# Optimization experiments

Measured on AMD Instinct MI355X. Metric: run time of the kernel, lower is better.

The kernel has to match this reference:

```python
import jax, jax.numpy as jnp
import numpy as np

B, S, D = 8, 2048, 1024
H = 2 * D  # FFN hidden
EPS = 1e-5

def _layernorm(x, gamma, beta):
    mu = jnp.mean(x, axis=-1, keepdims=True)
    var = jnp.mean(jnp.square(x - mu), axis=-1, keepdims=True)
    return (x - mu) * jax.lax.rsqrt(var + EPS) * gamma + beta

def setup_inputs() -> dict:
    key = jax.random.key(0)
    ks = jax.random.split(key, 9)
    s = 1.0 / np.sqrt(D)
    x = jax.random.normal(ks[0], (B, S, D), dtype=jnp.float32)
    Wq = jax.random.uniform(ks[1], (D, D), jnp.float32, -s, s)
    Wk = jax.random.uniform(ks[2], (D, D), jnp.float32, -s, s)
    Wv = jax.random.uniform(ks[3], (D, D), jnp.float32, -s, s)
    W1 = jax.random.uniform(ks[4], (H, D), jnp.float32, -s, s)
    b1 = jax.random.uniform(ks[5], (H,), jnp.float32, -s, s)
    s2 = 1.0 / np.sqrt(H)
    W2 = jax.random.uniform(ks[6], (D, H), jnp.float32, -s2, s2)
    b2 = jax.random.uniform(ks[7], (D,), jnp.float32, -s2, s2)
    g1 = jnp.ones((D,), jnp.float32); be1 = jnp.zeros((D,), jnp.float32)
    g2 = jnp.ones((D,), jnp.float32); be2 = jnp.zeros((D,), jnp.float32)
    return {"x": x, "Wq": Wq, "Wk": Wk, "Wv": Wv, "W1": W1, "b1": b1,
            "W2": W2, "b2": b2, "g1": g1, "be1": be1, "g2": g2, "be2": be2}

def reference(x, Wq, Wk, Wv, W1, b1, W2, b2, g1, be1, g2, be2):
    # q/k/v projections (torch Linear: x @ W.T)
    q = jnp.einsum('bsd,ed->bse', x, Wq)
    k = jnp.einsum('bsd,ed->bse', x, Wk)
    v = jnp.einsum('bsd,ed->bse', x, Wv)
    scores = jnp.einsum('bqd,bkd->bqk', q, k) / jnp.sqrt(jnp.float32(D))
    attn = jax.nn.softmax(scores, axis=-1)
    attn_out = jnp.einsum('bqk,bkd->bqd', attn, v)
    h = _layernorm(x + attn_out, g1, be1)
    ff = jnp.einsum('bsh,dh->bsd', jax.nn.relu(jnp.einsum('bsd,hd->bsh', h, W1) + b1), W2) + b2
    return _layernorm(h + ff, g2, be2)
```

## Files before the change

### kernel.cpp

```cpp
#include <hip/hip_runtime.h>
#include <hip/hip_bf16.h>


typedef __attribute__((ext_vector_type(4))) float  f32x4;
typedef __attribute__((ext_vector_type(8))) short  short8;
typedef __attribute__((ext_vector_type(4))) short  short4v;
typedef __attribute__((ext_vector_type(8))) __bf16 bf16x8;
typedef unsigned short ushort_t;

static __device__ __forceinline__ unsigned short f2bf(float f) {
  unsigned u = __builtin_bit_cast(unsigned, f);
  u += 0x7fffu + ((u >> 16) & 1u);
  return (unsigned short)(u >> 16);
}
static __device__ __forceinline__ float bf2f(unsigned short u) {
  return __builtin_bit_cast(float, (unsigned)u << 16);
}

#define GLDS16(g, l)                                                        \
  __builtin_amdgcn_global_load_lds(                                         \
      (const __attribute__((address_space(1))) void*)(g),                   \
      (__attribute__((address_space(3))) void*)(l), 16, 0, 0)

__global__ __launch_bounds__(256) void cvt_f32_bf16(
    const float* __restrict__ in, ushort_t* __restrict__ out, long n) {
  long i = ((long)blockIdx.x * 256 + threadIdx.x) * 8;
  if (i >= n) return;
  f32x4 a = *(const f32x4*)(in + i);
  f32x4 b = *(const f32x4*)(in + i + 4);
  short8 t;
  t[0] = (short)f2bf(a.x); t[1] = (short)f2bf(a.y);
  t[2] = (short)f2bf(a.z); t[3] = (short)f2bf(a.w);
  t[4] = (short)f2bf(b.x); t[5] = (short)f2bf(b.y);
  t[6] = (short)f2bf(b.z); t[7] = (short)f2bf(b.w);
  *(short8*)(out + i) = t;
}

enum { EP_QKV = 0, EP_BF16 = 1, EP_PV = 2, EP_FF1 = 3, EP_FF2 = 4 };

constexpr long BSDc = 8L * 2048 * 1024;

template <int EPI>
__global__ __launch_bounds__(512, 2) void gemm_bt(
    const ushort_t* __restrict__ A, const ushort_t* __restrict__ B,
    void* __restrict__ C, int N, int K, long sA, long sB, long sC, long sRes,
    const float* __restrict__ bias, const float* __restrict__ res,
    float scale) {
  __shared__ __align__(16) ushort_t As[2][2][8192];
  __shared__ __align__(16) ushort_t Bs[2][2][8192];
  const int tid  = threadIdx.x;
  const int lane = tid & 63;
  const int w    = tid >> 6;
  const int wm   = w >> 2;
  const int wn   = w & 3;
  const int l15  = lane & 15;
  const int hi   = lane >> 4;
  const long bz  = blockIdx.z;
  const long m0  = (long)blockIdx.x * 256;
  const long n0  = (long)blockIdx.y * 256;
  const ushort_t* Ab = A + bz * sA;
  const ushort_t* Bb = B + bz * sB;

  const int srow = tid >> 3;
  const int sc   = (tid & 7) ^ (srow & 7);
  const long offA0 = (m0 + srow) * (long)K + sc * 8;
  const long offB0 = (n0 + srow) * (long)K + sc * 8;
  const int dst0 = w * 512;
  const int dst1 = 4096 + w * 512;

#define STAGE_A(t, h)                                                       \
  {                                                                         \
    const long o_ = (long)(t) * 64 + (long)(h) * 128 * K;                   \
    ushort_t* l_ = &As[(t) & 1][h][0];                                      \
    GLDS16(Ab + offA0 + o_, l_ + dst0);                                     \
    GLDS16(Ab + offA0 + 64 * (long)K + o_, l_ + dst1);                      \
  }
#define STAGE_B(t, h)                                                       \
  {                                                                         \
    const long o_ = (long)(t) * 64 + (long)(h) * 128 * K;                   \
    ushort_t* l_ = &Bs[(t) & 1][h][0];                                      \
    GLDS16(Bb + offB0 + o_, l_ + dst0);                                     \
    GLDS16(Bb + offB0 + 64 * (long)K + o_, l_ + dst1);                      \
  }

  const int ab0 = l15 * 128 + ((hi) ^ (l15 & 7)) * 16;
  const int ab1 = l15 * 128 + ((4 + hi) ^ (l15 & 7)) * 16;

#define READ_A(ai)                                                          \
  _Pragma("unroll") for (int i = 0; i < 4; ++i) {                           \
    afr[i][0] = *(const short8*)(Ah + (ai) * 8192 + i * 2048 + ab0);        \
    afr[i][1] = *(const short8*)(Ah + (ai) * 8192 + i * 2048 + ab1);        \
  }
#define READ_B(bj)                                                          \
  _Pragma("unroll") for (int j = 0; j < 2; ++j) {                           \
    bfr[bj][j][0] = *(const short8*)(Bh + (bj) * 4096 + j * 2048 + ab0);    \
    bfr[bj][j][1] = *(const short8*)(Bh + (bj) * 4096 + j * 2048 + ab1);    \
  }
#define QMFMA(ib, jb, bsel)                                                 \
  _Pragma("unroll") for (int i = 0; i < 4; ++i)                             \
  _Pragma("unroll") for (int j = 0; j < 2; ++j)                             \
  _Pragma("unroll") for (int ks = 0; ks < 2; ++ks)                          \
    acc[(ib) + i][(jb) + j] = __builtin_amdgcn_mfma_f32_16x16x32_bf16(      \
        __builtin_bit_cast(bf16x8, afr[i][ks]),                             \
        __builtin_bit_cast(bf16x8, bfr[bsel][j][ks]),                       \
        acc[(ib) + i][(jb) + j], 0, 0, 0);

  f32x4 acc[8][4] = {};
  const int NT = K >> 6;

  STAGE_B(0, 0) STAGE_B(0, 1) STAGE_A(0, 0) STAGE_A(0, 1)
  STAGE_B(1, 0) STAGE_B(1, 1)
  asm volatile("s_waitcnt vmcnt(4)" ::: "memory");
  __builtin_amdgcn_sched_barrier(0);
  __builtin_amdgcn_s_barrier();
  __builtin_amdgcn_sched_barrier(0);

  for (int u = 0; u < NT; ++u) {
    const int d = u & 1;
    const char* Ah = (const char*)&As[d][wm][0];
    const char* Bh = (const char*)&Bs[d][wn >> 1][0] + (wn & 1) * 8192;
    short8 afr[4][2], bfr[2][2][2];
    READ_A(0)
    READ_B(0)
    if (u + 1 < NT) STAGE_A(u + 1, 0)
    __builtin_amdgcn_s_setprio(1);
    QMFMA(0, 0, 0)
    __builtin_amdgcn_s_setprio(0);
    READ_B(1)
    if (u + 1 < NT) STAGE_A(u + 1, 1)
    __builtin_amdgcn_s_setprio(1);
    QMFMA(0, 2, 1)
    __builtin_amdgcn_s_setprio(0);
    __builtin_amdgcn_s_barrier();
    READ_A(1)
    if (u + 2 < NT) STAGE_B(u + 2, 0)
    __builtin_amdgcn_s_setprio(1);
    QMFMA(4, 2, 1)
    __builtin_amdgcn_s_setprio(0);
    if (u + 2 < NT) STAGE_B(u + 2, 1)
    __builtin_amdgcn_s_setprio(1);
    QMFMA(4, 0, 0)
    __builtin_amdgcn_s_setprio(0);
    if (u + 1 < NT) {
      if (u + 2 < NT) {
        asm volatile("s_waitcnt vmcnt(4)" ::: "memory");
      } else {
        asm volatile("s_waitcnt vmcnt(0)" ::: "memory");
      }
      __builtin_amdgcn_sched_barrier(0);
      __builtin_amdgcn_s_barrier();
      __builtin_amdgcn_sched_barrier(0);
    }
  }
#undef STAGE_A
#undef STAGE_B
#undef READ_A
#undef READ_B
#undef QMFMA

  const int rb0 = hi << 2;
  const int cl  = l15;
#pragma unroll
  for (int i = 0; i < 8; ++i) {
#pragma unroll
    for (int j = 0; j < 4; ++j) {
      long gmb = m0 + wm * 128 + i * 16 + rb0;
      long gc  = n0 + wn * 64 + j * 16 + cl;
      if constexpr (EPI == EP_QKV) {
        long which = gc >> 10;
        long col   = gc & 1023;
        if (which == 2) {
          long bb = gmb >> 11, s = gmb & 2047;
          short4v pk;
#pragma unroll
          for (int r = 0; r < 4; ++r) pk[r] = (short)f2bf(acc[i][j][r]);
          *(short4v*)((ushort_t*)C + 2 * BSDc + ((bb << 10) + col) * 2048 + s) =
              pk;
        } else {
#pragma unroll
          for (int r = 0; r < 4; ++r)
            ((ushort_t*)C)[which * BSDc + (gmb + r) * 1024 + col] =
                f2bf(acc[i][j][r]);
        }
      } else {
#pragma unroll
        for (int r = 0; r < 4; ++r) {
          long gm = gmb + r;
          float v = acc[i][j][r] * scale;
          if constexpr (EPI == EP_BF16) {
            ((ushort_t*)C)[bz * sC + gm * N + gc] = f2bf(v);
          } else if constexpr (EPI == EP_PV) {
            v += res[bz * sRes + gm * N + gc];
            ((float*)C)[bz * sC + gm * N + gc] = v;
          } else if constexpr (EPI == EP_FF1) {
            v += bias[gc];
            v = v > 0.f ? v : 0.f;
            ((ushort_t*)C)[gm * N + gc] = f2bf(v);
          } else {
            v += bias[gc] + res[gm * N + gc];
            ((float*)C)[gm * N + gc] = v;
          }
        }
      }
    }
  }
}

__global__ __launch_bounds__(256) void softmax_inplace(
    ushort_t* __restrict__ P) {
  __shared__ float rmax[4], rsum[4];
  const int tid   = threadIdx.x;
  const long base = (long)blockIdx.x * 2048;
  short8 sv = *(const short8*)(P + base + tid * 8);
  float v[8];
#pragma unroll
  for (int j = 0; j < 8; ++j) v[j] = bf2f((unsigned short)sv[j]);
  float mx = v[0];
#pragma unroll
  for (int j = 1; j < 8; ++j) mx = fmaxf(mx, v[j]);
#pragma unroll
  for (int off = 32; off; off >>= 1) mx = fmaxf(mx, __shfl_down(mx, off, 64));
  if ((tid & 63) == 0) rmax[tid >> 6] = mx;
  __syncthreads();
  mx = fmaxf(fmaxf(rmax[0], rmax[1]), fmaxf(rmax[2], rmax[3]));
  float s = 0.f;
#pragma unroll
  for (int j = 0; j < 8; ++j) {
    v[j] = __expf(v[j] - mx);
    s += v[j];
  }
#pragma unroll
  for (int off = 32; off; off >>= 1) s += __shfl_down(s, off, 64);
  if ((tid & 63) == 0) rsum[tid >> 6] = s;
  __syncthreads();
  s = (rsum[0] + rsum[1]) + (rsum[2] + rsum[3]);
  float inv = 1.f / s;
  short8 o;
#pragma unroll
  for (int j = 0; j < 8; ++j) o[j] = (short)f2bf(v[j] * inv);
  *(short8*)(P + base + tid * 8) = o;
}

template <int MODE>
__global__ __launch_bounds__(256) void ln_row(const float* __restrict__ X,
                                              const float* __restrict__ g,
                                              const float* __restrict__ be,
                                              float* __restrict__ Yf,
                                              ushort_t* __restrict__ Yb) {
  __shared__ float rs[4], rq[4];
  const int tid   = threadIdx.x;
  const long base = (long)blockIdx.x << 10;
  f32x4 v = *(const f32x4*)(X + base + tid * 4);
  float s = v.x + v.y + v.z + v.w;
  float q = v.x * v.x + v.y * v.y + v.z * v.z + v.w * v.w;
#pragma unroll
  for (int off = 32; off; off >>= 1) {
    s += __shfl_down(s, off, 64);
    q += __shfl_down(q, off, 64);
  }
  if ((tid & 63) == 0) {
    rs[tid >> 6] = s;
    rq[tid >> 6] = q;
  }
  __syncthreads();
  s = (rs[0] + rs[1]) + (rs[2] + rs[3]);
  q = (rq[0] + rq[1]) + (rq[2] + rq[3]);
  float mu   = s * (1.f / 1024.f);
  float var  = q * (1.f / 1024.f) - mu * mu;
  float rstd = rsqrtf(var + 1e-5f);
  int c    = tid * 4;
  f32x4 gg = *(const f32x4*)(g + c);
  f32x4 bb = *(const f32x4*)(be + c);
  f32x4 y;
  y.x = (v.x - mu) * rstd * gg.x + bb.x;
  y.y = (v.y - mu) * rstd * gg.y + bb.y;
  y.z = (v.z - mu) * rstd * gg.z + bb.z;
  y.w = (v.w - mu) * rstd * gg.w + bb.w;
  *(f32x4*)(Yf + base + c) = y;
  if constexpr (MODE == 0) {
    short4v ob;
    ob[0] = (short)f2bf(y.x);
    ob[1] = (short)f2bf(y.y);
    ob[2] = (short)f2bf(y.z);
    ob[3] = (short)f2bf(y.w);
    *(short4v*)(Yb + base + c) = ob;
  }
}

extern "C" void kernel_launch(void* const* d_in, const int* in_sizes, int n_in,
                              void* d_out, int out_size, void* d_ws,
                              size_t ws_size, hipStream_t stream) {
  const float* x   = (const float*)d_in[0];
  const float* Wq  = (const float*)d_in[1];
  const float* Wk  = (const float*)d_in[2];
  const float* Wv  = (const float*)d_in[3];
  const float* W1  = (const float*)d_in[4];
  const float* b1  = (const float*)d_in[5];
  const float* W2  = (const float*)d_in[6];
  const float* b2  = (const float*)d_in[7];
  const float* g1  = (const float*)d_in[8];
  const float* be1 = (const float*)d_in[9];
  const float* g2  = (const float*)d_in[10];
  const float* be2 = (const float*)d_in[11];
  float* out = (float*)d_out;

  constexpr long BSD = 8L * 2048 * 1024;
  constexpr long BSS = 8L * 2048 * 2048;
  constexpr long DD  = 1024L * 1024;
  constexpr long HD  = 2048L * 1024;

  ushort_t* qb  = (ushort_t*)d_ws;
  ushort_t* kb  = qb + BSD;
  ushort_t* vTb = kb + BSD;
  ushort_t* sP  = vTb + BSD;
  float*    r1  = (float*)(sP + BSS);

  ushort_t* xb    = sP;
  ushort_t* Wqkvb = (ushort_t*)r1;
  ushort_t* W1b   = kb;
  ushort_t* W2b   = kb + HD;
  ushort_t* hb    = qb;
  float*    h     = out;

  dim3 blk(256), gblk(512);
  const long SD = 2048L * 1024, SS = 2048L * 2048, DS = 1024L * 2048;

  cvt_f32_bf16<<<dim3(8192), blk, 0, stream>>>(x, xb, BSD);
  cvt_f32_bf16<<<dim3(512), blk, 0, stream>>>(Wq, Wqkvb, DD);
  cvt_f32_bf16<<<dim3(512), blk, 0, stream>>>(Wk, Wqkvb + DD, DD);
  cvt_f32_bf16<<<dim3(512), blk, 0, stream>>>(Wv, Wqkvb + 2 * DD, DD);
  gemm_bt<EP_QKV><<<dim3(64, 12, 1), gblk, 0, stream>>>(
      xb, Wqkvb, qb, 3072, 1024, 0, 0, 0, 0, nullptr, nullptr, 1.f);
  gemm_bt<EP_BF16><<<dim3(8, 8, 8), gblk, 0, stream>>>(
      qb, kb, sP, 2048, 1024, SD, SD, SS, 0, nullptr, nullptr, 0.03125f);
  cvt_f32_bf16<<<dim3(1024), blk, 0, stream>>>(W1, W1b, HD);
  cvt_f32_bf16<<<dim3(1024), blk, 0, stream>>>(W2, W2b, HD);
  softmax_inplace<<<dim3(16384), blk, 0, stream>>>(sP);
  gemm_bt<EP_PV><<<dim3(8, 4, 8), gblk, 0, stream>>>(
      sP, vTb, r1, 1024, 2048, SS, DS, SD, SD, nullptr, x, 1.f);
  ln_row<0><<<dim3(16384), blk, 0, stream>>>(r1, g1, be1, h, hb);
  gemm_bt<EP_FF1><<<dim3(64, 8, 1), gblk, 0, stream>>>(
      hb, W1b, sP, 2048, 1024, 0, 0, 0, 0, b1, nullptr, 1.f);
  gemm_bt<EP_FF2><<<dim3(64, 4, 1), gblk, 0, stream>>>(
      sP, W2b, r1, 1024, 2048, 0, 0, 0, 0, b2, h, 1.f);
  ln_row<1><<<dim3(16384), blk, 0, stream>>>(r1, g2, be2, out, nullptr);
}
```

Baseline: 494.1 us.

## Switch GEMM inner loop from 16x16x32 to 32x32x16 bf16 MFMA tiles

Replaces the 16x16x32 bf16 MFMA instructions with 32x32x16 ones and rewrites the LDS fragment reads and the swizzle offsets to match the 32-row operand layout. It also remaps the epilogue to the 32x32 accumulator layout, where each lane holds 4 groups of 4 rows. Larger MFMA tiles cut the LDS reads per FLOP and the number of issued instructions. In exchange, each of the fewer wider instructions has a longer latency and the accumulator layout changes.

```diff
diff --git a/kernel.cpp b/kernel.cpp
--- a/kernel.cpp
+++ b/kernel.cpp
@@ -2,10 +2,11 @@
 #include <hip/hip_bf16.h>
 
 
-typedef __attribute__((ext_vector_type(4))) float  f32x4;
-typedef __attribute__((ext_vector_type(8))) short  short8;
-typedef __attribute__((ext_vector_type(4))) short  short4v;
-typedef __attribute__((ext_vector_type(8))) __bf16 bf16x8;
+typedef __attribute__((ext_vector_type(4))) float   f32x4;
+typedef __attribute__((ext_vector_type(16))) float  f32x16;
+typedef __attribute__((ext_vector_type(8))) short   short8;
+typedef __attribute__((ext_vector_type(4))) short   short4v;
+typedef __attribute__((ext_vector_type(8))) __bf16  bf16x8;
 typedef unsigned short ushort_t;
 
 static __device__ __forceinline__ unsigned short f2bf(float f) {
@@ -53,8 +54,9 @@
   const int w    = tid >> 6;
   const int wm   = w >> 2;
   const int wn   = w & 3;
-  const int l15  = lane & 15;
-  const int hi   = lane >> 4;
+  const int l31  = lane & 31;
+  const int hi1  = lane >> 5;
+  const int e    = lane & 7;
   const long bz  = blockIdx.z;
   const long m0  = (long)blockIdx.x * 256;
   const long n0  = (long)blockIdx.y * 256;
@@ -83,29 +85,28 @@
     GLDS16(Bb + offB0 + 64 * (long)K + o_, l_ + dst1);                      \
   }
 
-  const int ab0 = l15 * 128 + ((hi) ^ (l15 & 7)) * 16;
-  const int ab1 = l15 * 128 + ((4 + hi) ^ (l15 & 7)) * 16;
-
-#define READ_A(ai)                                                          \
-  _Pragma("unroll") for (int i = 0; i < 4; ++i) {                           \
-    afr[i][0] = *(const short8*)(Ah + (ai) * 8192 + i * 2048 + ab0);        \
-    afr[i][1] = *(const short8*)(Ah + (ai) * 8192 + i * 2048 + ab1);        \
-  }
-#define READ_B(bj)                                                          \
-  _Pragma("unroll") for (int j = 0; j < 2; ++j) {                           \
-    bfr[bj][j][0] = *(const short8*)(Bh + (bj) * 4096 + j * 2048 + ab0);    \
-    bfr[bj][j][1] = *(const short8*)(Bh + (bj) * 4096 + j * 2048 + ab1);    \
-  }
-#define QMFMA(ib, jb, bsel)                                                 \
-  _Pragma("unroll") for (int i = 0; i < 4; ++i)                             \
-  _Pragma("unroll") for (int j = 0; j < 2; ++j)                             \
-  _Pragma("unroll") for (int ks = 0; ks < 2; ++ks)                          \
-    acc[(ib) + i][(jb) + j] = __builtin_amdgcn_mfma_f32_16x16x32_bf16(      \
+  int sks[4];
+#pragma unroll
+  for (int ks = 0; ks < 4; ++ks) sks[ks] = (((2 * ks + hi1) ^ e) << 4);
+
+#define READ_A2(tb)                                                         \
+  _Pragma("unroll") for (int i = 0; i < 2; ++i)                             \
+  _Pragma("unroll") for (int ks = 0; ks < 4; ++ks)                          \
+    afr[i][ks] = *(const short8*)(Ah + (((tb) + i) * 32 + l31) * 128 +      \
+                                  sks[ks]);
+#define READ_B1(bj)                                                         \
+  _Pragma("unroll") for (int ks = 0; ks < 4; ++ks)                          \
+    bfr[bj][ks] = *(const short8*)(Bh + ((bj) * 32 + l31) * 128 + sks[ks]);
+
+#define QMFMA(ig, jt)                                                       \
+  _Pragma("unroll") for (int ks = 0; ks < 4; ++ks)                          \
+  _Pragma("unroll") for (int i = 0; i < 2; ++i)                             \
+    acc[(ig) * 2 + i][jt] = __builtin_amdgcn_mfma_f32_32x32x16_bf16(        \
         __builtin_bit_cast(bf16x8, afr[i][ks]),                             \
-        __builtin_bit_cast(bf16x8, bfr[bsel][j][ks]),                       \
-        acc[(ib) + i][(jb) + j], 0, 0, 0);
-
-  f32x4 acc[8][4] = {};
+        __builtin_bit_cast(bf16x8, bfr[jt][ks]), acc[(ig) * 2 + i][jt], 0,  \
+        0, 0);
+
+  f32x16 acc[4][2] = {};
   const int NT = K >> 6;
 
   STAGE_B(0, 0) STAGE_B(0, 1) STAGE_A(0, 0) STAGE_A(0, 1)
@@ -119,27 +120,27 @@
     const int d = u & 1;
     const char* Ah = (const char*)&As[d][wm][0];
     const char* Bh = (const char*)&Bs[d][wn >> 1][0] + (wn & 1) * 8192;
-    short8 afr[4][2], bfr[2][2][2];
-    READ_A(0)
-    READ_B(0)
+    short8 afr[2][4], bfr[2][4];
+    READ_A2(0)
+    READ_B1(0)
     if (u + 1 < NT) STAGE_A(u + 1, 0)
     __builtin_amdgcn_s_setprio(1);
-    QMFMA(0, 0, 0)
+    QMFMA(0, 0)
     __builtin_amdgcn_s_setprio(0);
-    READ_B(1)
+    READ_B1(1)
     if (u + 1 < NT) STAGE_A(u + 1, 1)
     __builtin_amdgcn_s_setprio(1);
-    QMFMA(0, 2, 1)
+    QMFMA(0, 1)
     __builtin_amdgcn_s_setprio(0);
     __builtin_amdgcn_s_barrier();
-    READ_A(1)
+    READ_A2(2)
     if (u + 2 < NT) STAGE_B(u + 2, 0)
     __builtin_amdgcn_s_setprio(1);
-    QMFMA(4, 2, 1)
+    QMFMA(1, 1)
     __builtin_amdgcn_s_setprio(0);
     if (u + 2 < NT) STAGE_B(u + 2, 1)
     __builtin_amdgcn_s_setprio(1);
-    QMFMA(4, 0, 0)
+    QMFMA(1, 0)
     __builtin_amdgcn_s_setprio(0);
     if (u + 1 < NT) {
       if (u + 2 < NT) {
@@ -154,51 +155,54 @@
   }
 #undef STAGE_A
 #undef STAGE_B
-#undef READ_A
-#undef READ_B
+#undef READ_A2
+#undef READ_B1
 #undef QMFMA
 
-  const int rb0 = hi << 2;
-  const int cl  = l15;
-#pragma unroll
-  for (int i = 0; i < 8; ++i) {
-#pragma unroll
-    for (int j = 0; j < 4; ++j) {
-      long gmb = m0 + wm * 128 + i * 16 + rb0;
-      long gc  = n0 + wn * 64 + j * 16 + cl;
-      if constexpr (EPI == EP_QKV) {
-        long which = gc >> 10;
-        long col   = gc & 1023;
-        if (which == 2) {
-          long bb = gmb >> 11, s = gmb & 2047;
-          short4v pk;
-#pragma unroll
-          for (int r = 0; r < 4; ++r) pk[r] = (short)f2bf(acc[i][j][r]);
-          *(short4v*)((ushort_t*)C + 2 * BSDc + ((bb << 10) + col) * 2048 + s) =
-              pk;
+#pragma unroll
+  for (int it = 0; it < 4; ++it) {
+#pragma unroll
+    for (int jt = 0; jt < 2; ++jt) {
+      const long rowb = m0 + wm * 128 + it * 32;
+      const long gc   = n0 + wn * 64 + jt * 32 + l31;
+#pragma unroll
+      for (int q = 0; q < 4; ++q) {
+        const long gr0 = rowb + 8 * q + 4 * hi1;
+        if constexpr (EPI == EP_QKV) {
+          long which = gc >> 10;
+          long col   = gc & 1023;
+          if (which == 2) {
+            long bb = gr0 >> 11, s = gr0 & 2047;
+            short4v pk;
+#pragma unroll
+            for (int r = 0; r < 4; ++r)
+              pk[r] = (short)f2bf(acc[it][jt][q * 4 + r]);
+            *(short4v*)((ushort_t*)C + 2 * BSDc + ((bb << 10) + col) * 2048 +
+                        s) = pk;
+          } else {
+#pragma unroll
+            for (int r = 0; r < 4; ++r)
+              ((ushort_t*)C)[which * BSDc + (gr0 + r) * 1024 + col] =
+                  f2bf(acc[it][jt][q * 4 + r]);
+          }
         } else {
 #pragma unroll
-          for (int r = 0; r < 4; ++r)
-            ((ushort_t*)C)[which * BSDc + (gmb + r) * 1024 + col] =
-                f2bf(acc[i][j][r]);
-        }
-      } else {
-#pragma unroll
-        for (int r = 0; r < 4; ++r) {
-          long gm = gmb + r;
-          float v = acc[i][j][r] * scale;
-          if constexpr (EPI == EP_BF16) {
-            ((ushort_t*)C)[bz * sC + gm * N + gc] = f2bf(v);
-          } else if constexpr (EPI == EP_PV) {
-            v += res[bz * sRes + gm * N + gc];
-            ((float*)C)[bz * sC + gm * N + gc] = v;
-          } else if constexpr (EPI == EP_FF1) {
-            v += bias[gc];
-            v = v > 0.f ? v : 0.f;
-            ((ushort_t*)C)[gm * N + gc] = f2bf(v);
-          } else {
-            v += bias[gc] + res[gm * N + gc];
-            ((float*)C)[gm * N + gc] = v;
+          for (int r = 0; r < 4; ++r) {
+            long gm = gr0 + r;
+            float v = acc[it][jt][q * 4 + r] * scale;
+            if constexpr (EPI == EP_BF16) {
+              ((ushort_t*)C)[bz * sC + gm * N + gc] = f2bf(v);
+            } else if constexpr (EPI == EP_PV) {
+              v += res[bz * sRes + gm * N + gc];
+              ((float*)C)[bz * sC + gm * N + gc] = v;
+            } else if constexpr (EPI == EP_FF1) {
+              v += bias[gc];
+              v = v > 0.f ? v : 0.f;
+              ((ushort_t*)C)[gm * N + gc] = f2bf(v);
+            } else {
+              v += bias[gc] + res[gm * N + gc];
+              ((float*)C)[gm * N + gc] = v;
+            }
           }
         }
       }
```

New measurement: 548.3 us. 1.11x slower.

## Use 1024-thread GEMM blocks with 16 waves each owning 64x64 tile

Applied to the files above, without the earlier changes.

The GEMM block grows from 512 to 1024 threads (16 waves), so each wave computes a 64x64 sub-tile instead of 128x64. Accumulator registers per wave are halved and each thread issues one global-to-LDS load per stage instead of two, with the vmcnt waits adjusted to match. The 256x256 block tile and LDS footprint stay the same. Occupancy drops to one block per CU, and each wave now loads its A fragment once per k-step with less MFMA work to hide that load behind. More waves also means more contention at the barriers.

```diff
diff --git a/kernel.cpp b/kernel.cpp
--- a/kernel.cpp
+++ b/kernel.cpp
@@ -41,7 +41,7 @@
 constexpr long BSDc = 8L * 2048 * 1024;
 
 template <int EPI>
-__global__ __launch_bounds__(512, 2) void gemm_bt(
+__global__ __launch_bounds__(1024, 1) void gemm_bt(
     const ushort_t* __restrict__ A, const ushort_t* __restrict__ B,
     void* __restrict__ C, int N, int K, long sA, long sB, long sC, long sRes,
     const float* __restrict__ bias, const float* __restrict__ res,
@@ -51,8 +51,8 @@
   const int tid  = threadIdx.x;
   const int lane = tid & 63;
   const int w    = tid >> 6;
-  const int wm   = w >> 2;
-  const int wn   = w & 3;
+  const int wm2  = w >> 2;
+  const int wn2  = w & 3;
   const int l15  = lane & 15;
   const int hi   = lane >> 4;
   const long bz  = blockIdx.z;
@@ -65,85 +65,71 @@
   const int sc   = (tid & 7) ^ (srow & 7);
   const long offA0 = (m0 + srow) * (long)K + sc * 8;
   const long offB0 = (n0 + srow) * (long)K + sc * 8;
-  const int dst0 = w * 512;
-  const int dst1 = 4096 + w * 512;
+  const int dst = (w << 9);
 
 #define STAGE_A(t, h)                                                       \
-  {                                                                         \
-    const long o_ = (long)(t) * 64 + (long)(h) * 128 * K;                   \
-    ushort_t* l_ = &As[(t) & 1][h][0];                                      \
-    GLDS16(Ab + offA0 + o_, l_ + dst0);                                     \
-    GLDS16(Ab + offA0 + 64 * (long)K + o_, l_ + dst1);                      \
-  }
+  GLDS16(Ab + offA0 + (long)(t) * 64 + (long)(h) * 128 * K,                 \
+         &As[(t) & 1][h][0] + dst);
 #define STAGE_B(t, h)                                                       \
-  {                                                                         \
-    const long o_ = (long)(t) * 64 + (long)(h) * 128 * K;                   \
-    ushort_t* l_ = &Bs[(t) & 1][h][0];                                      \
-    GLDS16(Bb + offB0 + o_, l_ + dst0);                                     \
-    GLDS16(Bb + offB0 + 64 * (long)K + o_, l_ + dst1);                      \
-  }
+  GLDS16(Bb + offB0 + (long)(t) * 64 + (long)(h) * 128 * K,                 \
+         &Bs[(t) & 1][h][0] + dst);
 
   const int ab0 = l15 * 128 + ((hi) ^ (l15 & 7)) * 16;
   const int ab1 = l15 * 128 + ((4 + hi) ^ (l15 & 7)) * 16;
 
-#define READ_A(ai)                                                          \
+#define READ_A_ALL                                                          \
   _Pragma("unroll") for (int i = 0; i < 4; ++i) {                           \
-    afr[i][0] = *(const short8*)(Ah + (ai) * 8192 + i * 2048 + ab0);        \
-    afr[i][1] = *(const short8*)(Ah + (ai) * 8192 + i * 2048 + ab1);        \
-  }
-#define READ_B(bj)                                                          \
-  _Pragma("unroll") for (int j = 0; j < 2; ++j) {                           \
-    bfr[bj][j][0] = *(const short8*)(Bh + (bj) * 4096 + j * 2048 + ab0);    \
-    bfr[bj][j][1] = *(const short8*)(Bh + (bj) * 4096 + j * 2048 + ab1);    \
-  }
-#define QMFMA(ib, jb, bsel)                                                 \
+    afr[i][0] = *(const short8*)(Ah + i * 2048 + ab0);                      \
+    afr[i][1] = *(const short8*)(Ah + i * 2048 + ab1);                      \
+  }
+#define READ_B2(bj0)                                                        \
+  _Pragma("unroll") for (int jj = 0; jj < 2; ++jj) {                        \
+    bfr[jj][0] = *(const short8*)(Bh + ((bj0) + jj) * 2048 + ab0);          \
+    bfr[jj][1] = *(const short8*)(Bh + ((bj0) + jj) * 2048 + ab1);          \
+  }
+#define QMFMA(jb)                                                           \
   _Pragma("unroll") for (int i = 0; i < 4; ++i)                             \
-  _Pragma("unroll") for (int j = 0; j < 2; ++j)                             \
+  _Pragma("unroll") for (int jj = 0; jj < 2; ++jj)                          \
   _Pragma("unroll") for (int ks = 0; ks < 2; ++ks)                          \
-    acc[(ib) + i][(jb) + j] = __builtin_amdgcn_mfma_f32_16x16x32_bf16(      \
+    acc[i][(jb) + jj] = __builtin_amdgcn_mfma_f32_16x16x32_bf16(            \
         __builtin_bit_cast(bf16x8, afr[i][ks]),                             \
-        __builtin_bit_cast(bf16x8, bfr[bsel][j][ks]),                       \
-        acc[(ib) + i][(jb) + j], 0, 0, 0);
-
-  f32x4 acc[8][4] = {};
+        __builtin_bit_cast(bf16x8, bfr[jj][ks]), acc[i][(jb) + jj], 0, 0,   \
+        0);
+
+  f32x4 acc[4][4] = {};
   const int NT = K >> 6;
 
   STAGE_B(0, 0) STAGE_B(0, 1) STAGE_A(0, 0) STAGE_A(0, 1)
   STAGE_B(1, 0) STAGE_B(1, 1)
-  asm volatile("s_waitcnt vmcnt(4)" ::: "memory");
+  asm volatile("s_waitcnt vmcnt(2)" ::: "memory");
   __builtin_amdgcn_sched_barrier(0);
   __builtin_amdgcn_s_barrier();
   __builtin_amdgcn_sched_barrier(0);
 
   for (int u = 0; u < NT; ++u) {
     const int d = u & 1;
-    const char* Ah = (const char*)&As[d][wm][0];
-    const char* Bh = (const char*)&Bs[d][wn >> 1][0] + (wn & 1) * 8192;
-    short8 afr[4][2], bfr[2][2][2];
-    READ_A(0)
-    READ_B(0)
+    const char* Ah = (const char*)&As[d][wm2 >> 1][0] + (wm2 & 1) * 8192;
+    const char* Bh = (const char*)&Bs[d][wn2 >> 1][0] + (wn2 & 1) * 8192;
+    short8 afr[4][2], bfr[2][2];
+    READ_A_ALL
+    READ_B2(0)
     if (u + 1 < NT) STAGE_A(u + 1, 0)
     __builtin_amdgcn_s_setprio(1);
-    QMFMA(0, 0, 0)
+    QMFMA(0)
     __builtin_amdgcn_s_setprio(0);
-    READ_B(1)
+    READ_B2(2)
     if (u + 1 < NT) STAGE_A(u + 1, 1)
     __builtin_amdgcn_s_setprio(1);
-    QMFMA(0, 2, 1)
+    QMFMA(2)
     __builtin_amdgcn_s_setprio(0);
     __builtin_amdgcn_s_barrier();
-    READ_A(1)
-    if (u + 2 < NT) STAGE_B(u + 2, 0)
-    __builtin_amdgcn_s_setprio(1);
-    QMFMA(4, 2, 1)
-    __builtin_amdgcn_s_setprio(0);
-    if (u + 2 < NT) STAGE_B(u + 2, 1)
-    __builtin_amdgcn_s_setprio(1);
-    QMFMA(4, 0, 0)
-    __builtin_amdgcn_s_setprio(0);
+    if (u + 2 < NT) {
+      STAGE_B(u + 2, 0)
+      STAGE_B(u + 2, 1)
+    }
     if (u + 1 < NT) {
       if (u + 2 < NT) {
-        asm volatile("s_waitcnt vmcnt(4)" ::: "memory");
+        asm volatile("s_waitcnt vmcnt(2)" ::: "memory");
       } else {
         asm volatile("s_waitcnt vmcnt(0)" ::: "memory");
       }
@@ -154,18 +140,18 @@
   }
 #undef STAGE_A
 #undef STAGE_B
-#undef READ_A
-#undef READ_B
+#undef READ_A_ALL
+#undef READ_B2
 #undef QMFMA
 
   const int rb0 = hi << 2;
   const int cl  = l15;
 #pragma unroll
-  for (int i = 0; i < 8; ++i) {
+  for (int i = 0; i < 4; ++i) {
 #pragma unroll
     for (int j = 0; j < 4; ++j) {
-      long gmb = m0 + wm * 128 + i * 16 + rb0;
-      long gc  = n0 + wn * 64 + j * 16 + cl;
+      long gmb = m0 + wm2 * 64 + i * 16 + rb0;
+      long gc  = n0 + wn2 * 64 + j * 16 + cl;
       if constexpr (EPI == EP_QKV) {
         long which = gc >> 10;
         long col   = gc & 1023;
@@ -322,7 +308,7 @@
   ushort_t* hb    = qb;
   float*    h     = out;
 
-  dim3 blk(256), gblk(512);
+  dim3 blk(256), gblk(1024);
   const long SD = 2048L * 1024, SS = 2048L * 2048, DS = 1024L * 2048;
 
   cvt_f32_bf16<<<dim3(8192), blk, 0, stream>>>(x, xb, BSD);
```

New measurement: 613.7 us. 24.2% more time.
